# Kernel tuning notes

Hardware: AMD Instinct MI355X
Metric: run time of the kernel (lower is better)

Reference implementation:

```python
import jax, jax.numpy as jnp
import numpy as np

IN_F, OUT_F = 2048, 2048
N_EXPERTS, RANK, TOP_K = 8, 128, 2


def setup_inputs() -> dict:
    key = jax.random.key(0)
    k_x, k_r, k_a, k_b = jax.random.split(key, 4)
    hidden_states = jax.random.normal(k_x, (4, 4096, IN_F), dtype=jnp.float32)
    # router_proj.weight is [E, in]; we store it transposed so logits = x @ router_w
    router_w = jax.random.normal(k_r, (IN_F, N_EXPERTS), dtype=jnp.float32) * (IN_F ** -0.5)
    # expert e: a_proj [in, rank], b_proj [rank, out] (transposed nn.Linear weights)
    Wa = jax.random.normal(k_a, (N_EXPERTS, IN_F, RANK), dtype=jnp.float32) * (IN_F ** -0.5)
    Wb = jax.random.normal(k_b, (N_EXPERTS, RANK, OUT_F), dtype=jnp.float32) * (RANK ** -0.5)
    return {"hidden_states": hidden_states, "router_w": router_w, "Wa": Wa, "Wb": Wb}


def reference(hidden_states, router_w, Wa, Wb):
    B, S, D = hidden_states.shape
    x = hidden_states.reshape(-1, D)  # [T, in]
    # F.normalize(x, dim=-1): x / max(||x||_2, 1e-12)
    norm = jnp.maximum(jnp.linalg.norm(x, axis=-1, keepdims=True), 1e-12)
    router_logits = (x / norm) @ router_w  # [T, E]
    routing_weights = jax.nn.softmax(router_logits.astype(jnp.float32), axis=-1)
    rw, selected_experts = jax.lax.top_k(routing_weights, TOP_K)  # [T, k]
    rw = rw / jnp.sum(rw, axis=-1, keepdims=True)
    rw = rw.astype(hidden_states.dtype)
    # combine[t, e] = routing weight if expert e selected for token t, else 0.
    combine = jnp.sum(jax.nn.one_hot(selected_experts, N_EXPERTS, dtype=rw.dtype) * rw[..., None], axis=1)  # [T, E]
    out = jnp.zeros((x.shape[0], OUT_F), dtype=hidden_states.dtype)
    for e in range(N_EXPERTS):  # small fixed expert count
        out = out + combine[:, e, None] * ((x @ Wa[e]) @ Wb[e])
    return out.reshape(B, S, OUT_F)
```

## Files before the change

kernel.cpp:

```cpp
#include <hip/hip_runtime.h>
#include <cstdint>
#include <cstddef>

#define TOKENS 16384
#define DIM    2048
#define NEXP   8
#define RANK   128
#define NOUT   2048
#define CAP    8192

typedef __attribute__((ext_vector_type(4))) float    f32x4;
typedef __attribute__((ext_vector_type(8))) _Float16 f16x8;
typedef __attribute__((ext_vector_type(4))) _Float16 f16x4;

__device__ __forceinline__ void gload_lds16(const void* g, void* l) {
  __builtin_amdgcn_global_load_lds(
      (const __attribute__((address_space(1))) void*)g,
      (__attribute__((address_space(3))) void*)l, 16, 0, 0);
}

__global__ __launch_bounds__(256) void transpose_cast_f16(
    const float* __restrict__ in, _Float16* __restrict__ out,
    int R, int C, long ostride, long obase)
{
  __shared__ float tile[32][33];
  const int e = blockIdx.z;
  const float* ine = in + (size_t)e * R * C;
  const int c0 = blockIdx.x * 32, r0 = blockIdx.y * 32;
  const int tx = threadIdx.x, ty = threadIdx.y;
#pragma unroll
  for (int j = 0; j < 32; j += 8)
    tile[ty + j][tx] = ine[(size_t)(r0 + ty + j) * C + (c0 + tx)];
  __syncthreads();
#pragma unroll
  for (int j = 0; j < 32; j += 8)
    out[(size_t)e * obase + (size_t)(c0 + ty + j) * ostride + (r0 + tx)] =
        (_Float16)tile[tx][ty + j];
}

__global__ __launch_bounds__(256) void logits_fused_kernel(
    const float* __restrict__ x, const float* __restrict__ rw,
    float* __restrict__ lgpart, float* __restrict__ ssqpart,
    _Float16* __restrict__ xh)
{
  __shared__ __align__(16) char lds[65536];
  char* ldsA  = lds;
  char* ldsBh = lds + 32768;
  char* ldsBe = lds + 49152;
  const int tid = threadIdx.x;
  const int w = tid >> 6, l = tid & 63;
  const int m0 = blockIdx.x * 128;
  const int ks = blockIdx.y;
  const int kbase = ks * 512;

#pragma unroll
  for (int i = 0; i < 32; ++i) {
    const int idx = tid * 32 + i;
    const int n = idx >> 9, k = idx & 511;
    const float v = (n < 8) ? rw[(size_t)(kbase + k) * 8 + n] : 0.f;
    const _Float16 h = (_Float16)v;
    const _Float16 e = (_Float16)(v - (float)h);
    const int off = n * 1024 + ((k * 2) ^ ((n & 7) << 4));
    *(_Float16*)(ldsBh + off) = h;
    *(_Float16*)(ldsBe + off) = e;
  }

  const int Lb = w * 1024 + l * 16;
  const float* agp[8];
  int ldst[8];
#pragma unroll
  for (int i = 0; i < 8; ++i) {
    const int L = i * 4096 + Lb;
    const int row = L >> 8;
    const int cb = (L & 255) ^ ((row & 7) << 4);
    agp[i] = x + (size_t)(m0 + row) * DIM + kbase + (cb >> 2);
    ldst[i] = i * 4096 + w * 1024;
  }

  f32x4 acc[2];
  float ssl[2] = {0.f, 0.f};
#pragma unroll
  for (int mf = 0; mf < 2; ++mf)
#pragma unroll
    for (int j = 0; j < 4; ++j) acc[mf][j] = 0.f;

  for (int st = 0; st < 8; ++st) {
#pragma unroll
    for (int i = 0; i < 8; ++i)
      gload_lds16(agp[i] + st * 64, ldsA + ldst[i]);
    __syncthreads();
#pragma unroll
    for (int kk = 0; kk < 2; ++kk) {
      const int n = l & 15;
      const int bko = n * 1024 +
          ((st * 128 + kk * 64 + ((l >> 4) << 4)) ^ ((n & 7) << 4));
      const f16x8 bh = *(const f16x8*)(ldsBh + bko);
      const f16x8 be = *(const f16x8*)(ldsBe + bko);
#pragma unroll
      for (int mf = 0; mf < 2; ++mf) {
        const int r = w * 32 + mf * 16 + (l & 15);
        const int s = (r & 7) << 4;
        const int c0 = kk * 128 + ((l >> 4) << 5);
        const f32x4 va = *(const f32x4*)(ldsA + r * 256 + ((c0) ^ s));
        const f32x4 vb = *(const f32x4*)(ldsA + r * 256 + ((c0 + 16) ^ s));
        float f[8] = {va[0], va[1], va[2], va[3], vb[0], vb[1], vb[2], vb[3]};
        f16x8 ah, ae;
#pragma unroll
        for (int j = 0; j < 8; ++j) {
          ah[j] = (_Float16)f[j];
          ae[j] = (_Float16)(f[j] - (float)ah[j]);
          ssl[mf] = fmaf(f[j], f[j], ssl[mf]);
        }
        *(f16x8*)(xh + (size_t)(m0 + r) * DIM + kbase + st * 64 + kk * 32 +
                  ((l >> 4) << 3)) = ah;
        acc[mf] = __builtin_amdgcn_mfma_f32_16x16x32_f16(ae, bh, acc[mf], 0, 0, 0);
        acc[mf] = __builtin_amdgcn_mfma_f32_16x16x32_f16(ah, be, acc[mf], 0, 0, 0);
        acc[mf] = __builtin_amdgcn_mfma_f32_16x16x32_f16(ah, bh, acc[mf], 0, 0, 0);
      }
    }
    __syncthreads();
  }

  const int col = l & 15;
  if (col < 8) {
#pragma unroll
    for (int mf = 0; mf < 2; ++mf) {
      const int rbase = m0 + w * 32 + mf * 16 + ((l >> 4) << 2);
#pragma unroll
      for (int j = 0; j < 4; ++j)
        lgpart[((size_t)ks * TOKENS + rbase + j) * 8 + col] = acc[mf][j];
    }
  }
#pragma unroll
  for (int mf = 0; mf < 2; ++mf) {
    float s = ssl[mf];
    s += __shfl_xor(s, 16, 64);
    s += __shfl_xor(s, 32, 64);
    if (l < 16)
      ssqpart[(size_t)ks * TOKENS + m0 + w * 32 + mf * 16 + l] = s;
  }
}

__global__ __launch_bounds__(256) void softmax_top2_kernel(
    const float* __restrict__ lgpart, const float* __restrict__ ssqpart,
    float* __restrict__ combine, int* __restrict__ pairinfo,
    int* __restrict__ counts, unsigned short* __restrict__ ids16)
{
  const size_t t = (size_t)blockIdx.x * 256 + threadIdx.x;
  float ss = 0.f;
  float lg[8];
#pragma unroll
  for (int e = 0; e < 8; ++e) lg[e] = 0.f;
#pragma unroll
  for (int ks = 0; ks < 4; ++ks) {
    ss += ssqpart[(size_t)ks * TOKENS + t];
    const float* p = lgpart + ((size_t)ks * TOKENS + t) * 8;
    float4 a = *(const float4*)(p);
    float4 b = *(const float4*)(p + 4);
    lg[0] += a.x; lg[1] += a.y; lg[2] += a.z; lg[3] += a.w;
    lg[4] += b.x; lg[5] += b.y; lg[6] += b.z; lg[7] += b.w;
  }
  const float iv = 1.f / fmaxf(sqrtf(ss), 1e-12f);
#pragma unroll
  for (int e = 0; e < 8; ++e) lg[e] *= iv;
  float b1 = lg[0]; int e1 = 0;
#pragma unroll
  for (int e = 1; e < 8; ++e)
    if (lg[e] > b1) { b1 = lg[e]; e1 = e; }
  float b2 = -3.4e38f; int e2 = 0;
#pragma unroll
  for (int e = 0; e < 8; ++e)
    if (e != e1 && lg[e] > b2) { b2 = lg[e]; e2 = e; }
  const float p2 = expf(b2 - b1);
  const float w1 = 1.f / (1.f + p2);
  const float w2 = p2 * w1;
  float ov[8];
#pragma unroll
  for (int e = 0; e < 8; ++e)
    ov[e] = (e == e1) ? w1 : ((e == e2) ? w2 : 0.f);
  float4* cp = (float4*)(combine + t * 8);
  cp[0] = make_float4(ov[0], ov[1], ov[2], ov[3]);
  cp[1] = make_float4(ov[4], ov[5], ov[6], ov[7]);

  const int a = min(e1, e2), b = max(e1, e2);
  pairinfo[t] = a | (b << 8);
  const int bin = a * 8 + b;
  const int pos = atomicAdd(&counts[bin], 1);
  if (pos < CAP) ids16[bin * CAP + pos] = (unsigned short)t;
}

__global__ void make_items_kernel(const int* __restrict__ counts,
                                  int4* __restrict__ items)
{
  if (threadIdx.x == 0 && blockIdx.x == 0) {
    int j = 0;
    for (int b = 0; b < 64; ++b) {
      int c = counts[b]; if (c > CAP) c = CAP;
      for (int s = 0; s < c; s += 128)
        items[j++] = make_int4(b, b * CAP + s, min(128, c - s), 0);
    }
    for (; j < 192; ++j) items[j] = make_int4(-1, 0, 0, 0);
  }
}

__global__ __launch_bounds__(256) void gemm1_pair_kernel(
    const _Float16* __restrict__ xh, const _Float16* __restrict__ WaT,
    const float* __restrict__ combine, const unsigned short* __restrict__ ids,
    const int4* __restrict__ items, _Float16* __restrict__ Yc)
{
  __shared__ __align__(16) char lds[32768];
  __shared__ int ids_lds[128];
  char* ldsA = lds;
  char* ldsB = lds + 16384;
  const int4 item = items[blockIdx.y];
  if (item.x < 0) return;
  const int slot = blockIdx.x;
  const int e = slot ? (item.x & 7) : (item.x >> 3);
  const int tid = threadIdx.x;
  const int w = tid >> 6, l = tid & 63;
  const int wm = w >> 1, wn = w & 1;

  if (tid < 128)
    ids_lds[tid] = (tid < item.z) ? (int)ids[item.y + tid] : -1;
  __syncthreads();

  const int Lb = w * 1024 + l * 16;
  const _Float16* aptr[4];
  const _Float16* bptr[4];
  int ldst[4];
#pragma unroll
  for (int i = 0; i < 4; ++i) {
    const int L = i * 4096 + Lb;
    const int row = L >> 7;
    const int cb = (L & 127) ^ ((row & 7) << 4);
    int t = ids_lds[row]; if (t < 0) t = 0;
    aptr[i] = xh + (size_t)t * DIM + (cb >> 1);
    bptr[i] = WaT + (size_t)(e * 128 + row) * DIM + (cb >> 1);
    ldst[i] = i * 4096 + w * 1024;
  }

  f32x4 acc[4][4];
#pragma unroll
  for (int p = 0; p < 4; ++p)
#pragma unroll
    for (int q = 0; q < 4; ++q)
#pragma unroll
      for (int j = 0; j < 4; ++j) acc[p][q][j] = 0.f;

  for (int kt = 0; kt < DIM; kt += 64) {
#pragma unroll
    for (int i = 0; i < 4; ++i) {
      gload_lds16(aptr[i] + kt, ldsA + ldst[i]);
      gload_lds16(bptr[i] + kt, ldsB + ldst[i]);
    }
    __syncthreads();
#pragma unroll
    for (int kk = 0; kk < 2; ++kk) {
      const int kb = kk * 64 + ((l >> 4) << 4);
      f16x8 af[4], bfr[4];
#pragma unroll
      for (int mf = 0; mf < 4; ++mf) {
        const int r = (wm << 6) + (mf << 4) + (l & 15);
        af[mf] = *(const f16x8*)(ldsA + r * 128 + (kb ^ ((r & 7) << 4)));
      }
#pragma unroll
      for (int nf = 0; nf < 4; ++nf) {
        const int r = (wn << 6) + (nf << 4) + (l & 15);
        bfr[nf] = *(const f16x8*)(ldsB + r * 128 + (kb ^ ((r & 7) << 4)));
      }
#pragma unroll
      for (int mf = 0; mf < 4; ++mf)
#pragma unroll
        for (int nf = 0; nf < 4; ++nf)
          acc[mf][nf] = __builtin_amdgcn_mfma_f32_16x16x32_f16(
              af[mf], bfr[nf], acc[mf][nf], 0, 0, 0);
    }
    __syncthreads();
  }

  const int cr = (l >> 4) << 2;
  const int cc = l & 15;
#pragma unroll
  for (int mf = 0; mf < 4; ++mf) {
    const int lr0 = (wm << 6) + (mf << 4) + cr;
#pragma unroll
    for (int j = 0; j < 4; ++j) {
      const int t = ids_lds[lr0 + j];
      if (t < 0) continue;
      const float cs = combine[(size_t)t * 8 + e];
      _Float16* yr = Yc + (size_t)t * 256 + slot * 128;
#pragma unroll
      for (int nf = 0; nf < 4; ++nf)
        yr[(wn << 6) + (nf << 4) + cc] = (_Float16)(acc[mf][nf][j] * cs);
    }
  }
}

__global__ __launch_bounds__(256) void gemm2_pair_kernel(
    const _Float16* __restrict__ Y, const _Float16* __restrict__ WbT,
    const unsigned short* __restrict__ ids, const int4* __restrict__ items,
    float* __restrict__ out)
{
  __shared__ __align__(16) char lds[32768];
  __shared__ int ids_lds[128];
  char* ldsA = lds;
  char* ldsB = lds + 16384;
  const int4 item = items[blockIdx.y];
  if (item.x < 0) return;
  const int a = item.x >> 3, b = item.x & 7;
  const int n0 = blockIdx.x * 128;
  const int tid = threadIdx.x;
  const int w = tid >> 6, l = tid & 63;
  const int wm = w >> 1, wn = w & 1;

  if (tid < 128)
    ids_lds[tid] = (tid < item.z) ? (int)ids[item.y + tid] : -1;
  __syncthreads();

  const int Lb = w * 1024 + l * 16;
  const _Float16* aptr[4];
  const _Float16* bptrA[4];
  const _Float16* bptrB[4];
  int ldst[4];
#pragma unroll
  for (int i = 0; i < 4; ++i) {
    const int L = i * 4096 + Lb;
    const int row = L >> 7;
    const int cb = (L & 127) ^ ((row & 7) << 4);
    int t = ids_lds[row]; if (t < 0) t = 0;
    aptr[i]  = Y + (size_t)t * 256 + (cb >> 1);
    bptrA[i] = WbT + (size_t)(n0 + row) * 1024 + a * 128 + (cb >> 1);
    bptrB[i] = WbT + (size_t)(n0 + row) * 1024 + b * 128 + (cb >> 1);
    ldst[i] = i * 4096 + w * 1024;
  }

  f32x4 acc[4][4];
#pragma unroll
  for (int p = 0; p < 4; ++p)
#pragma unroll
    for (int q = 0; q < 4; ++q)
#pragma unroll
      for (int j = 0; j < 4; ++j) acc[p][q][j] = 0.f;

#pragma unroll
  for (int kt = 0; kt < 4; ++kt) {
#pragma unroll
    for (int i = 0; i < 4; ++i) {
      gload_lds16(aptr[i] + kt * 64, ldsA + ldst[i]);
      const _Float16* bs = (kt < 2) ? (bptrA[i] + kt * 64)
                                    : (bptrB[i] + (kt - 2) * 64);
      gload_lds16(bs, ldsB + ldst[i]);
    }
    __syncthreads();
#pragma unroll
    for (int kk = 0; kk < 2; ++kk) {
      const int kb = kk * 64 + ((l >> 4) << 4);
      f16x8 af[4], bfr[4];
#pragma unroll
      for (int mf = 0; mf < 4; ++mf) {
        const int r = (wm << 6) + (mf << 4) + (l & 15);
        af[mf] = *(const f16x8*)(ldsA + r * 128 + (kb ^ ((r & 7) << 4)));
      }
#pragma unroll
      for (int nf = 0; nf < 4; ++nf) {
        const int r = (wn << 6) + (nf << 4) + (l & 15);
        bfr[nf] = *(const f16x8*)(ldsB + r * 128 + (kb ^ ((r & 7) << 4)));
      }
#pragma unroll
      for (int mf = 0; mf < 4; ++mf)
#pragma unroll
        for (int nf = 0; nf < 4; ++nf)
          acc[mf][nf] = __builtin_amdgcn_mfma_f32_16x16x32_f16(
              af[mf], bfr[nf], acc[mf][nf], 0, 0, 0);
    }
    __syncthreads();
  }

  const int cr = (l >> 4) << 2;
  const int cc = l & 15;
#pragma unroll
  for (int mf = 0; mf < 4; ++mf) {
    const int lr0 = (wm << 6) + (mf << 4) + cr;
#pragma unroll
    for (int j = 0; j < 4; ++j) {
      const int t = ids_lds[lr0 + j];
      if (t < 0) continue;
      float* orow = out + (size_t)t * NOUT + n0;
#pragma unroll
      for (int nf = 0; nf < 4; ++nf)
        orow[(wn << 6) + (nf << 4) + cc] = acc[mf][nf][j];
    }
  }
}

extern "C" void kernel_launch(void* const* d_in, const int* in_sizes, int n_in,
                              void* d_out, int out_size, void* d_ws, size_t ws_size,
                              hipStream_t stream) {
  const float* x  = (const float*)d_in[0];
  const float* rw = (const float*)d_in[1];
  const float* Wa = (const float*)d_in[2];
  const float* Wb = (const float*)d_in[3];
  float* out = (float*)d_out;

  char* ws = (char*)d_ws;
  _Float16* xh       = (_Float16*)(ws);
  _Float16* WaT      = (_Float16*)(ws + 67108864);
  _Float16* WbT      = (_Float16*)(ws + 71303168);
  float*    combine  = (float*)   (ws + 75497472);
  int*      pairinfo = (int*)     (ws + 76021760);
  int*      counts   = (int*)     (ws + 76087296);
  int4*     items    = (int4*)    (ws + 76087552);
  unsigned short* ids16 = (unsigned short*)(ws + 76090624);
  _Float16* Yc       = (_Float16*)(ws + 77139200);
  float*    lgpart   = (float*)   (ws + 77139200);
  float*    ssqpart  = (float*)   (ws + 79236352);

  transpose_cast_f16<<<dim3(4, 64, 8), dim3(32, 8), 0, stream>>>(
      Wa, WaT, 2048, 128, 2048, (long)128 * 2048);
  transpose_cast_f16<<<dim3(64, 4, 8), dim3(32, 8), 0, stream>>>(
      Wb, WbT, 128, 2048, 1024, 128);

  logits_fused_kernel<<<dim3(TOKENS / 128, 4), 256, 0, stream>>>(
      x, rw, lgpart, ssqpart, xh);

  hipMemsetAsync(counts, 0, 64 * sizeof(int), stream);
  softmax_top2_kernel<<<TOKENS / 256, 256, 0, stream>>>(
      lgpart, ssqpart, combine, pairinfo, counts, ids16);
  make_items_kernel<<<1, 64, 0, stream>>>(counts, items);

  gemm1_pair_kernel<<<dim3(2, 192), 256, 0, stream>>>(
      xh, WaT, combine, ids16, items, Yc);
  gemm2_pair_kernel<<<dim3(NOUT / 128, 192), 256, 0, stream>>>(
      Yc, WbT, ids16, items, out);
}
```

Measured before the change: 200.1 us.

## Load router-logit activations directly from global and double the K-split

The fused logits/norm/cast kernel stops staging x tiles in LDS through async global-to-LDS loads with barriers and instead reads each lane's float fragments straight from global memory. The K range is split into 8 slices instead of 4, so the grid doubles, and LDS per block shrinks to 16 KB. The aim is higher occupancy and no per-stage barriers, at the cost of less coalesced direct loads. The softmax kernel also has to sum 8 partials, which adds partial-buffer traffic.

```diff
diff --git a/kernel.cpp b/kernel.cpp
--- a/kernel.cpp
+++ b/kernel.cpp
@@ -8,6 +8,7 @@
 #define RANK   128
 #define NOUT   2048
 #define CAP    8192
+#define KSL    8
 
 typedef __attribute__((ext_vector_type(4))) float    f32x4;
 typedef __attribute__((ext_vector_type(8))) _Float16 f16x8;
@@ -43,39 +44,27 @@
     float* __restrict__ lgpart, float* __restrict__ ssqpart,
     _Float16* __restrict__ xh)
 {
-  __shared__ __align__(16) char lds[65536];
-  char* ldsA  = lds;
-  char* ldsBh = lds + 32768;
-  char* ldsBe = lds + 49152;
+  __shared__ __align__(16) char lds[16384];
+  char* ldsBh = lds;
+  char* ldsBe = lds + 8192;
   const int tid = threadIdx.x;
   const int w = tid >> 6, l = tid & 63;
   const int m0 = blockIdx.x * 128;
   const int ks = blockIdx.y;
-  const int kbase = ks * 512;
-
-#pragma unroll
-  for (int i = 0; i < 32; ++i) {
-    const int idx = tid * 32 + i;
-    const int n = idx >> 9, k = idx & 511;
+  const int kbase = ks * 256;
+
+#pragma unroll
+  for (int i = 0; i < 16; ++i) {
+    const int idx = tid * 16 + i;
+    const int n = idx >> 8, k = idx & 255;
     const float v = (n < 8) ? rw[(size_t)(kbase + k) * 8 + n] : 0.f;
     const _Float16 h = (_Float16)v;
     const _Float16 e = (_Float16)(v - (float)h);
-    const int off = n * 1024 + ((k * 2) ^ ((n & 7) << 4));
+    const int off = n * 512 + ((k * 2) ^ ((n & 7) << 4));
     *(_Float16*)(ldsBh + off) = h;
     *(_Float16*)(ldsBe + off) = e;
   }
-
-  const int Lb = w * 1024 + l * 16;
-  const float* agp[8];
-  int ldst[8];
-#pragma unroll
-  for (int i = 0; i < 8; ++i) {
-    const int L = i * 4096 + Lb;
-    const int row = L >> 8;
-    const int cb = (L & 255) ^ ((row & 7) << 4);
-    agp[i] = x + (size_t)(m0 + row) * DIM + kbase + (cb >> 2);
-    ldst[i] = i * 4096 + w * 1024;
-  }
+  __syncthreads();
 
   f32x4 acc[2];
   float ssl[2] = {0.f, 0.f};
@@ -84,25 +73,21 @@
 #pragma unroll
     for (int j = 0; j < 4; ++j) acc[mf][j] = 0.f;
 
-  for (int st = 0; st < 8; ++st) {
-#pragma unroll
-    for (int i = 0; i < 8; ++i)
-      gload_lds16(agp[i] + st * 64, ldsA + ldst[i]);
-    __syncthreads();
+  for (int st = 0; st < 4; ++st) {
 #pragma unroll
     for (int kk = 0; kk < 2; ++kk) {
       const int n = l & 15;
-      const int bko = n * 1024 +
+      const int bko = n * 512 +
           ((st * 128 + kk * 64 + ((l >> 4) << 4)) ^ ((n & 7) << 4));
       const f16x8 bh = *(const f16x8*)(ldsBh + bko);
       const f16x8 be = *(const f16x8*)(ldsBe + bko);
+      const int c = kbase + st * 64 + kk * 32 + ((l >> 4) << 3);
 #pragma unroll
       for (int mf = 0; mf < 2; ++mf) {
-        const int r = w * 32 + mf * 16 + (l & 15);
-        const int s = (r & 7) << 4;
-        const int c0 = kk * 128 + ((l >> 4) << 5);
-        const f32x4 va = *(const f32x4*)(ldsA + r * 256 + ((c0) ^ s));
-        const f32x4 vb = *(const f32x4*)(ldsA + r * 256 + ((c0 + 16) ^ s));
+        const int r = m0 + w * 32 + mf * 16 + (l & 15);
+        const float* xp = x + (size_t)r * DIM + c;
+        const f32x4 va = *(const f32x4*)(xp);
+        const f32x4 vb = *(const f32x4*)(xp + 4);
         float f[8] = {va[0], va[1], va[2], va[3], vb[0], vb[1], vb[2], vb[3]};
         f16x8 ah, ae;
 #pragma unroll
@@ -111,14 +96,12 @@
           ae[j] = (_Float16)(f[j] - (float)ah[j]);
           ssl[mf] = fmaf(f[j], f[j], ssl[mf]);
         }
-        *(f16x8*)(xh + (size_t)(m0 + r) * DIM + kbase + st * 64 + kk * 32 +
-                  ((l >> 4) << 3)) = ah;
+        *(f16x8*)(xh + (size_t)r * DIM + c) = ah;
         acc[mf] = __builtin_amdgcn_mfma_f32_16x16x32_f16(ae, bh, acc[mf], 0, 0, 0);
         acc[mf] = __builtin_amdgcn_mfma_f32_16x16x32_f16(ah, be, acc[mf], 0, 0, 0);
         acc[mf] = __builtin_amdgcn_mfma_f32_16x16x32_f16(ah, bh, acc[mf], 0, 0, 0);
       }
     }
-    __syncthreads();
   }
 
   const int col = l & 15;
@@ -152,7 +135,7 @@
 #pragma unroll
   for (int e = 0; e < 8; ++e) lg[e] = 0.f;
 #pragma unroll
-  for (int ks = 0; ks < 4; ++ks) {
+  for (int ks = 0; ks < KSL; ++ks) {
     ss += ssqpart[(size_t)ks * TOKENS + t];
     const float* p = lgpart + ((size_t)ks * TOKENS + t) * 8;
     float4 a = *(const float4*)(p);
@@ -413,14 +396,14 @@
   unsigned short* ids16 = (unsigned short*)(ws + 76090624);
   _Float16* Yc       = (_Float16*)(ws + 77139200);
   float*    lgpart   = (float*)   (ws + 77139200);
-  float*    ssqpart  = (float*)   (ws + 79236352);
+  float*    ssqpart  = (float*)   (ws + 81333504);
 
   transpose_cast_f16<<<dim3(4, 64, 8), dim3(32, 8), 0, stream>>>(
       Wa, WaT, 2048, 128, 2048, (long)128 * 2048);
   transpose_cast_f16<<<dim3(64, 4, 8), dim3(32, 8), 0, stream>>>(
       Wb, WbT, 128, 2048, 1024, 128);
 
-  logits_fused_kernel<<<dim3(TOKENS / 128, 4), 256, 0, stream>>>(
+  logits_fused_kernel<<<dim3(TOKENS / 128, KSL), 256, 0, stream>>>(
       x, rw, lgpart, ssqpart, xh);
 
   hipMemsetAsync(counts, 0, 64 * sizeof(int), stream);
```

Result: slower. 219.0 us (+9.4%).

## Halve gemm1 token tile to 64 rows and build items with a parallel scan

Applied to the files above, without the earlier changes.

The first expert GEMM now takes 64-token tiles instead of 128, so it launches twice as many blocks (384 instead of 192). This gives better CU occupancy and less padding waste for small pair bins. The item-list builder becomes a wave-parallel prefix scan that emits separate 64-row and 128-row item lists, replacing the single-thread loop. The unused pairinfo buffer is removed. In exchange, each gemm1 block does less MFMA work per B-tile load, so reuse of the Wa weight tile is halved.

```diff
diff --git a/kernel.cpp b/kernel.cpp
--- a/kernel.cpp
+++ b/kernel.cpp
@@ -8,6 +8,7 @@
 #define RANK   128
 #define NOUT   2048
 #define CAP    8192
+#define KSL    4
 
 typedef __attribute__((ext_vector_type(4))) float    f32x4;
 typedef __attribute__((ext_vector_type(8))) _Float16 f16x8;
@@ -143,8 +144,8 @@
 
 __global__ __launch_bounds__(256) void softmax_top2_kernel(
     const float* __restrict__ lgpart, const float* __restrict__ ssqpart,
-    float* __restrict__ combine, int* __restrict__ pairinfo,
-    int* __restrict__ counts, unsigned short* __restrict__ ids16)
+    float* __restrict__ combine, int* __restrict__ counts,
+    unsigned short* __restrict__ ids16)
 {
   const size_t t = (size_t)blockIdx.x * 256 + threadIdx.x;
   float ss = 0.f;
@@ -152,7 +153,7 @@
 #pragma unroll
   for (int e = 0; e < 8; ++e) lg[e] = 0.f;
 #pragma unroll
-  for (int ks = 0; ks < 4; ++ks) {
+  for (int ks = 0; ks < KSL; ++ks) {
     ss += ssqpart[(size_t)ks * TOKENS + t];
     const float* p = lgpart + ((size_t)ks * TOKENS + t) * 8;
     float4 a = *(const float4*)(p);
@@ -183,24 +184,35 @@
   cp[1] = make_float4(ov[4], ov[5], ov[6], ov[7]);
 
   const int a = min(e1, e2), b = max(e1, e2);
-  pairinfo[t] = a | (b << 8);
   const int bin = a * 8 + b;
   const int pos = atomicAdd(&counts[bin], 1);
   if (pos < CAP) ids16[bin * CAP + pos] = (unsigned short)t;
 }
 
 __global__ void make_items_kernel(const int* __restrict__ counts,
-                                  int4* __restrict__ items)
-{
-  if (threadIdx.x == 0 && blockIdx.x == 0) {
-    int j = 0;
-    for (int b = 0; b < 64; ++b) {
-      int c = counts[b]; if (c > CAP) c = CAP;
-      for (int s = 0; s < c; s += 128)
-        items[j++] = make_int4(b, b * CAP + s, min(128, c - s), 0);
-    }
-    for (; j < 192; ++j) items[j] = make_int4(-1, 0, 0, 0);
-  }
+                                  int4* __restrict__ items64,
+                                  int4* __restrict__ items128)
+{
+  const int l = threadIdx.x;
+  const int c = min(counts[l], CAP);
+  const int n64 = (c + 63) >> 6;
+  const int n128 = (c + 127) >> 7;
+  int p64 = n64, p128 = n128;
+#pragma unroll
+  for (int m = 1; m < 64; m <<= 1) {
+    int u = __shfl_up(p64, m, 64);  if (l >= m) p64 += u;
+    int v = __shfl_up(p128, m, 64); if (l >= m) p128 += v;
+  }
+  const int tot64 = __shfl(p64, 63, 64);
+  const int tot128 = __shfl(p128, 63, 64);
+  int j = p64 - n64;
+  for (int s = 0; s < c; s += 64, ++j)
+    items64[j] = make_int4(l, l * CAP + s, min(64, c - s), 0);
+  j = p128 - n128;
+  for (int s = 0; s < c; s += 128, ++j)
+    items128[j] = make_int4(l, l * CAP + s, min(128, c - s), 0);
+  for (int k = tot64 + l; k < 384; k += 64) items64[k] = make_int4(-1, 0, 0, 0);
+  for (int k = tot128 + l; k < 192; k += 64) items128[k] = make_int4(-1, 0, 0, 0);
 }
 
 __global__ __launch_bounds__(256) void gemm1_pair_kernel(
@@ -208,10 +220,10 @@
     const float* __restrict__ combine, const unsigned short* __restrict__ ids,
     const int4* __restrict__ items, _Float16* __restrict__ Yc)
 {
-  __shared__ __align__(16) char lds[32768];
-  __shared__ int ids_lds[128];
+  __shared__ __align__(16) char lds[24576];
+  __shared__ int ids_lds[64];
   char* ldsA = lds;
-  char* ldsB = lds + 16384;
+  char* ldsB = lds + 8192;
   const int4 item = items[blockIdx.y];
   if (item.x < 0) return;
   const int slot = blockIdx.x;
@@ -220,28 +232,35 @@
   const int w = tid >> 6, l = tid & 63;
   const int wm = w >> 1, wn = w & 1;
 
-  if (tid < 128)
+  if (tid < 64)
     ids_lds[tid] = (tid < item.z) ? (int)ids[item.y + tid] : -1;
   __syncthreads();
 
   const int Lb = w * 1024 + l * 16;
-  const _Float16* aptr[4];
+  const _Float16* aptr[2];
   const _Float16* bptr[4];
-  int ldst[4];
-#pragma unroll
-  for (int i = 0; i < 4; ++i) {
+  int ldstA[2], ldstB[4];
+#pragma unroll
+  for (int i = 0; i < 2; ++i) {
     const int L = i * 4096 + Lb;
     const int row = L >> 7;
     const int cb = (L & 127) ^ ((row & 7) << 4);
     int t = ids_lds[row]; if (t < 0) t = 0;
     aptr[i] = xh + (size_t)t * DIM + (cb >> 1);
+    ldstA[i] = i * 4096 + w * 1024;
+  }
+#pragma unroll
+  for (int i = 0; i < 4; ++i) {
+    const int L = i * 4096 + Lb;
+    const int row = L >> 7;
+    const int cb = (L & 127) ^ ((row & 7) << 4);
     bptr[i] = WaT + (size_t)(e * 128 + row) * DIM + (cb >> 1);
-    ldst[i] = i * 4096 + w * 1024;
-  }
-
-  f32x4 acc[4][4];
-#pragma unroll
-  for (int p = 0; p < 4; ++p)
+    ldstB[i] = i * 4096 + w * 1024;
+  }
+
+  f32x4 acc[2][4];
+#pragma unroll
+  for (int p = 0; p < 2; ++p)
 #pragma unroll
     for (int q = 0; q < 4; ++q)
 #pragma unroll
@@ -249,18 +268,19 @@
 
   for (int kt = 0; kt < DIM; kt += 64) {
 #pragma unroll
-    for (int i = 0; i < 4; ++i) {
-      gload_lds16(aptr[i] + kt, ldsA + ldst[i]);
-      gload_lds16(bptr[i] + kt, ldsB + ldst[i]);
-    }
+    for (int i = 0; i < 2; ++i)
+      gload_lds16(aptr[i] + kt, ldsA + ldstA[i]);
+#pragma unroll
+    for (int i = 0; i < 4; ++i)
+      gload_lds16(bptr[i] + kt, ldsB + ldstB[i]);
     __syncthreads();
 #pragma unroll
     for (int kk = 0; kk < 2; ++kk) {
       const int kb = kk * 64 + ((l >> 4) << 4);
-      f16x8 af[4], bfr[4];
-#pragma unroll
-      for (int mf = 0; mf < 4; ++mf) {
-        const int r = (wm << 6) + (mf << 4) + (l & 15);
+      f16x8 af[2], bfr[4];
+#pragma unroll
+      for (int mf = 0; mf < 2; ++mf) {
+        const int r = (wm << 5) + (mf << 4) + (l & 15);
         af[mf] = *(const f16x8*)(ldsA + r * 128 + (kb ^ ((r & 7) << 4)));
       }
 #pragma unroll
@@ -269,7 +289,7 @@
         bfr[nf] = *(const f16x8*)(ldsB + r * 128 + (kb ^ ((r & 7) << 4)));
       }
 #pragma unroll
-      for (int mf = 0; mf < 4; ++mf)
+      for (int mf = 0; mf < 2; ++mf)
 #pragma unroll
         for (int nf = 0; nf < 4; ++nf)
           acc[mf][nf] = __builtin_amdgcn_mfma_f32_16x16x32_f16(
@@ -281,17 +301,17 @@
   const int cr = (l >> 4) << 2;
   const int cc = l & 15;
 #pragma unroll
-  for (int mf = 0; mf < 4; ++mf) {
-    const int lr0 = (wm << 6) + (mf << 4) + cr;
+  for (int mf = 0; mf < 2; ++mf) {
+    const int lr0 = (wm << 5) + (mf << 4) + cr;
 #pragma unroll
     for (int j = 0; j < 4; ++j) {
       const int t = ids_lds[lr0 + j];
       if (t < 0) continue;
       const float cs = combine[(size_t)t * 8 + e];
-      _Float16* yr = Yc + (size_t)t * 256 + slot * 128;
+      _Float16* yr = Yc + (size_t)t * 256 + slot * 128 + (wn << 6);
 #pragma unroll
       for (int nf = 0; nf < 4; ++nf)
-        yr[(wn << 6) + (nf << 4) + cc] = (_Float16)(acc[mf][nf][j] * cs);
+        yr[(nf << 4) + cc] = (_Float16)(acc[mf][nf][j] * cs);
     }
   }
 }
@@ -407,29 +427,29 @@
   _Float16* WaT      = (_Float16*)(ws + 67108864);
   _Float16* WbT      = (_Float16*)(ws + 71303168);
   float*    combine  = (float*)   (ws + 75497472);
-  int*      pairinfo = (int*)     (ws + 76021760);
-  int*      counts   = (int*)     (ws + 76087296);
-  int4*     items    = (int4*)    (ws + 76087552);
-  unsigned short* ids16 = (unsigned short*)(ws + 76090624);
-  _Float16* Yc       = (_Float16*)(ws + 77139200);
-  float*    lgpart   = (float*)   (ws + 77139200);
-  float*    ssqpart  = (float*)   (ws + 79236352);
+  int*      counts   = (int*)     (ws + 76021760);
+  int4*     items64  = (int4*)    (ws + 76022016);
+  int4*     items128 = (int4*)    (ws + 76028160);
+  unsigned short* ids16 = (unsigned short*)(ws + 76031232);
+  _Float16* Yc       = (_Float16*)(ws + 77079808);
+  float*    lgpart   = (float*)   (ws + 77079808);
+  float*    ssqpart  = (float*)   (ws + 79177728);
 
   transpose_cast_f16<<<dim3(4, 64, 8), dim3(32, 8), 0, stream>>>(
       Wa, WaT, 2048, 128, 2048, (long)128 * 2048);
   transpose_cast_f16<<<dim3(64, 4, 8), dim3(32, 8), 0, stream>>>(
       Wb, WbT, 128, 2048, 1024, 128);
 
-  logits_fused_kernel<<<dim3(TOKENS / 128, 4), 256, 0, stream>>>(
+  logits_fused_kernel<<<dim3(TOKENS / 128, KSL), 256, 0, stream>>>(
       x, rw, lgpart, ssqpart, xh);
 
   hipMemsetAsync(counts, 0, 64 * sizeof(int), stream);
   softmax_top2_kernel<<<TOKENS / 256, 256, 0, stream>>>(
-      lgpart, ssqpart, combine, pairinfo, counts, ids16);
-  make_items_kernel<<<1, 64, 0, stream>>>(counts, items);
-
-  gemm1_pair_kernel<<<dim3(2, 192), 256, 0, stream>>>(
-      xh, WaT, combine, ids16, items, Yc);
+      lgpart, ssqpart, combine, counts, ids16);
+  make_items_kernel<<<1, 64, 0, stream>>>(counts, items64, items128);
+
+  gemm1_pair_kernel<<<dim3(2, 384), 256, 0, stream>>>(
+      xh, WaT, combine, ids16, items64, Yc);
   gemm2_pair_kernel<<<dim3(NOUT / 128, 192), 256, 0, stream>>>(
-      Yc, WbT, ids16, items, out);
-}
+      Yc, WbT, ids16, items128, out);
+}
```

Measured after the change: 183.3 us. -8.4%, faster.
